# Performance work log

Hardware: AMD Instinct MI355X
Metric: run time of the kernel (lower is better)

The kernel has to match this reference:

```python
import jax, jax.numpy as jnp
import numpy as np

NUM_CHOICES = 12
NUM_LAYERS = 32
LSTM_SIZE = 2048
TEMPERATURE = 5.0
TANH_CONSTANT = 2.5


def setup_inputs() -> dict:
    key = jax.random.key(0)
    ks = jax.random.split(key, 6)
    H, C = LSTM_SIZE, NUM_CHOICES
    u = lambda k, shape: jax.random.uniform(k, shape, jnp.float32, -0.1, 0.1)
    return {
        "prev_c": jnp.zeros((1, H), jnp.float32),
        "prev_h": jnp.zeros((1, H), jnp.float32),
        "encoder": u(ks[0], (C, H)),
        "w_ih": u(ks[1], (4 * H, H)),
        "w_hh": u(ks[2], (4 * H, H)),
        "b_ih": u(ks[3], (4 * H,)),
        "b_hh": u(ks[4], (4 * H,)),
        "w_soft": u(ks[5], (C, H)),
    }


def _rollout(prev_c, prev_h, encoder, w_ih, w_hh, b_ih, b_hh, w_soft):
    keys = jax.random.split(jax.random.key(42), NUM_LAYERS)
    x0 = encoder[0][None, :]  # inputs = encoder(zeros(1).long())

    def step(carry, key):
        c, h, x = carry
        # torch LSTMCell: gates = x W_ih^T + b_ih + h W_hh^T + b_hh; order i,f,g,o
        gates = x @ w_ih.T + b_ih + h @ w_hh.T + b_hh  # [1, 4H]
        i, f, g, o = jnp.split(gates, 4, axis=-1)
        c2 = jax.nn.sigmoid(f) * c + jax.nn.sigmoid(i) * jnp.tanh(g)
        h2 = jax.nn.sigmoid(o) * jnp.tanh(c2)
        logits = (h2 @ w_soft.T) / TEMPERATURE
        logits = TANH_CONSTANT * jnp.tanh(logits)  # [1, C]
        logp = jax.nn.log_softmax(logits, axis=-1)
        op = jax.random.categorical(key, logits[0])  # scalar int, ~ multinomial(prob,1)
        nll = -logp[0, op]  # F.cross_entropy(logits, op_id), batch=1
        ent = jax.lax.stop_gradient(-jnp.sum(jnp.exp(logp) * logp))
        x_next = encoder[op + 1][None, :]  # note: op+1 gather (clamped at table edge)
        return (c2, h2, x_next), (op, nll, ent)

    (_, _, _), (op_seq, nlls, ents) = jax.lax.scan(step, (prev_c, prev_h, x0), keys)
    return op_seq, jnp.sum(nlls), jnp.sum(ents)


def reference(prev_c, prev_h, encoder, w_ih, w_hh, b_ih, b_hh, w_soft):
    return _rollout(prev_c, prev_h, encoder, w_ih, w_hh, b_ih, b_hh, w_soft)
```

## Files before the change

### kernel.cpp

```cpp
#include <hip/hip_runtime.h>
#include <stdint.h>

#define HDIM 2048
#define NC   12
#define NL   32
#define NBLK 256
#define NTHR 512
#define NWAVE 8
#define SPINCAP 2000000
#define TAG(t) (0x600D0000u | (uint32_t)(t))

__device__ __forceinline__ uint32_t rotl32(uint32_t x, int r) {
  return (x << r) | (x >> (32 - r));
}
__device__ __forceinline__ void tf2x32(uint32_t k0, uint32_t k1,
                                       uint32_t &x0, uint32_t &x1) {
  const uint32_t ks2 = k0 ^ k1 ^ 0x1BD11BDAu;
  x0 += k0; x1 += k1;
#define TFR(r) { x0 += x1; x1 = rotl32(x1, (r)); x1 ^= x0; }
  TFR(13) TFR(15) TFR(26) TFR(6)   x0 += k1;  x1 += ks2 + 1u;
  TFR(17) TFR(29) TFR(16) TFR(24)  x0 += ks2; x1 += k0  + 2u;
  TFR(13) TFR(15) TFR(26) TFR(6)   x0 += k0;  x1 += k1  + 3u;
  TFR(17) TFR(29) TFR(16) TFR(24)  x0 += k1;  x1 += ks2 + 4u;
  TFR(13) TFR(15) TFR(26) TFR(6)   x0 += ks2; x1 += k0  + 5u;
#undef TFR
}

__device__ __forceinline__ uint64_t ald64(const uint64_t* p) {
  return __hip_atomic_load(p, __ATOMIC_RELAXED, __HIP_MEMORY_SCOPE_AGENT);
}
__device__ __forceinline__ void ast64(uint64_t* p, uint64_t v) {
  __hip_atomic_store(p, v, __ATOMIC_RELAXED, __HIP_MEMORY_SCOPE_AGENT);
}
#define CFENCE() asm volatile("" ::: "memory")

__global__ void __launch_bounds__(NTHR, 2) ctrl_kernel(
    const float* __restrict__ prev_c, const float* __restrict__ prev_h,
    const float* __restrict__ encoder, const float* __restrict__ w_ih,
    const float* __restrict__ w_hh, const float* __restrict__ b_ih,
    const float* __restrict__ b_hh, const float* __restrict__ w_soft,
    float* __restrict__ out, float* __restrict__ ws)
{
  const int tid  = threadIdx.x;
  const int lane = tid & 63;
  const int wv   = tid >> 6;
  const int blk  = blockIdx.x;
  const int j    = blk * NWAVE + wv;

  uint64_t* hb = (uint64_t*)ws;

  __shared__ __align__(16) float s_h[HDIM];
  __shared__ float s_E[NWAVE][4][NC];
  __shared__ float s_dot[16];
  __shared__ int   s_op;

  if (tid < 16) s_dot[tid] = 0.f;

  {
    float4 wif[4][8];
    #pragma unroll
    for (int g = 0; g < 4; ++g) {
      const float4* wp = reinterpret_cast<const float4*>(w_ih + (size_t)(g * HDIM + j) * HDIM);
      #pragma unroll
      for (int k = 0; k < 8; ++k) wif[g][k] = wp[k * 64 + lane];
    }
    float bsum[4];
    #pragma unroll
    for (int g = 0; g < 4; ++g) bsum[g] = b_ih[g * HDIM + j] + b_hh[g * HDIM + j];

    for (int c = 0; c < NC; ++c) {
      const float4* ep = reinterpret_cast<const float4*>(encoder + (size_t)c * HDIM);
      float s0 = 0.f, s1 = 0.f, s2 = 0.f, s3 = 0.f;
      #pragma unroll
      for (int k = 0; k < 8; ++k) {
        float4 e = ep[k * 64 + lane];
        s0 += wif[0][k].x*e.x + wif[0][k].y*e.y + wif[0][k].z*e.z + wif[0][k].w*e.w;
        s1 += wif[1][k].x*e.x + wif[1][k].y*e.y + wif[1][k].z*e.z + wif[1][k].w*e.w;
        s2 += wif[2][k].x*e.x + wif[2][k].y*e.y + wif[2][k].z*e.z + wif[2][k].w*e.w;
        s3 += wif[3][k].x*e.x + wif[3][k].y*e.y + wif[3][k].z*e.z + wif[3][k].w*e.w;
      }
      #pragma unroll
      for (int d = 1; d < 64; d <<= 1) {
        s0 += __shfl_xor(s0, d, 64); s1 += __shfl_xor(s1, d, 64);
        s2 += __shfl_xor(s2, d, 64); s3 += __shfl_xor(s3, d, 64);
      }
      if (lane == 0) {
        s_E[wv][0][c] = s0 + bsum[0]; s_E[wv][1][c] = s1 + bsum[1];
        s_E[wv][2][c] = s2 + bsum[2]; s_E[wv][3][c] = s3 + bsum[3];
      }
    }
  }
  __syncthreads();

  float c_val   = prev_c[j];
  float nll_acc = 0.f, ent_acc = 0.f;

  for (int t = 0; t <= NL; ++t) {
    if (t == 0) {
      reinterpret_cast<float4*>(s_h)[tid] = reinterpret_cast<const float4*>(prev_h)[tid];
    } else {
      const uint64_t* base = hb + ((t - 1) & 1) * HDIM + wv * 256;
      const uint32_t want = TAG(t - 1);
      uint64_t v0 = 0, v1 = 0, v2 = 0, v3 = 0;
      for (int it = 0; it < SPINCAP; ++it) {
        v0 = ald64(base + lane);       v1 = ald64(base + lane + 64);
        v2 = ald64(base + lane + 128); v3 = ald64(base + lane + 192);
        bool ok = ((uint32_t)(v0 >> 32) == want) & ((uint32_t)(v1 >> 32) == want)
                & ((uint32_t)(v2 >> 32) == want) & ((uint32_t)(v3 >> 32) == want);
        if (__all(ok)) break;
      }
      CFENCE();
      s_h[wv * 256 + lane]       = __uint_as_float((uint32_t)v0);
      s_h[wv * 256 + lane + 64]  = __uint_as_float((uint32_t)v1);
      s_h[wv * 256 + lane + 128] = __uint_as_float((uint32_t)v2);
      s_h[wv * 256 + lane + 192] = __uint_as_float((uint32_t)v3);
    }
    __syncthreads();

    if (t > 0) {
      const int c0 = wv, c1 = wv + 8;
      const float4* sh4 = reinterpret_cast<const float4*>(s_h);
      const float4* wsA = reinterpret_cast<const float4*>(w_soft + (size_t)c0 * HDIM);
      const float4* wsB = reinterpret_cast<const float4*>(w_soft + (size_t)(c1 < NC ? c1 : 0) * HDIM);
      float d0 = 0.f, d1 = 0.f;
      #pragma unroll
      for (int k = 0; k < 8; ++k) {
        float4 h4 = sh4[k * 64 + lane];
        float4 a  = wsA[k * 64 + lane];
        d0 += a.x*h4.x + a.y*h4.y + a.z*h4.z + a.w*h4.w;
        if (c1 < NC) {
          float4 b = wsB[k * 64 + lane];
          d1 += b.x*h4.x + b.y*h4.y + b.z*h4.z + b.w*h4.w;
        }
      }
      #pragma unroll
      for (int d = 1; d < 64; d <<= 1) {
        d0 += __shfl_xor(d0, d, 64);
        d1 += __shfl_xor(d1, d, 64);
      }
      if (lane == 0) {
        s_dot[c0] = d0;
        if (c1 < NC) s_dot[c1] = d1;
      }
    }
    __syncthreads();

    if (t > 0 && wv == 0) {
      const int tt = t - 1;
      const float logit = (lane < NC) ? 2.5f * tanhf(s_dot[lane] * 0.2f) : 0.f;

      uint32_t k0, k1, bits;
      { uint32_t a = 0u, b = (uint32_t)tt;   tf2x32(0u, 42u, a, b); k0 = a; k1 = b; }
      { uint32_t a = 0u, b = (uint32_t)lane; tf2x32(k0, k1, a, b); bits = a ^ b; }
      const float TINY = 1.175494350822287508e-38f;
      float f01 = __uint_as_float((bits >> 9) | 0x3f800000u) - 1.0f;
      float u = f01 * (1.0f - TINY) + TINY;
      u = fmaxf(TINY, u);
      const float gmb = -logf(-logf(u));

      float by = (lane < NC) ? (logit + gmb) : -1e30f;
      int   bi = (lane < NC) ? lane : 999;
      #pragma unroll
      for (int d = 1; d < 16; d <<= 1) {
        float oy = __shfl_xor(by, d, 16);
        int   oi = __shfl_xor(bi, d, 16);
        if (oy > by || (oy == by && oi < bi)) { by = oy; bi = oi; }
      }
      const int op = bi;

      if (blk == 0) {
        float m = (lane < NC) ? logit : -1e30f;
        #pragma unroll
        for (int d = 1; d < 16; d <<= 1) m = fmaxf(m, __shfl_xor(m, d, 16));
        const float sh = logit - m;
        float S = (lane < NC) ? expf(sh) : 0.f;
        #pragma unroll
        for (int d = 1; d < 16; d <<= 1) S += __shfl_xor(S, d, 16);
        const float lp = sh - logf(S);
        const float lp_op = __shfl(lp, op, 16);
        float tm = (lane < NC) ? expf(lp) * lp : 0.f;
        #pragma unroll
        for (int d = 1; d < 16; d <<= 1) tm += __shfl_xor(tm, d, 16);
        if (lane == 0) {
          out[tt] = (float)op + 0.002f;
          nll_acc += -lp_op;
          ent_acc += -tm;
          if (t == NL) { out[NL] = nll_acc; out[NL + 1] = ent_acc; }
        }
      }
      if (lane == 0) s_op = op;
    }
    if (t == NL) break;

    float4 hf[8];
    #pragma unroll
    for (int k = 0; k < 8; ++k) hf[k] = reinterpret_cast<const float4*>(s_h)[k * 64 + lane];
    float gate[4];
    #pragma unroll
    for (int g = 0; g < 4; ++g) {
      const float4* wp = reinterpret_cast<const float4*>(w_hh + (size_t)(g * HDIM + j) * HDIM);
      float s = 0.f;
      #pragma unroll
      for (int k = 0; k < 8; ++k) {
        float4 b = wp[k * 64 + lane];
        s += b.x*hf[k].x + b.y*hf[k].y + b.z*hf[k].z + b.w*hf[k].w;
      }
      #pragma unroll
      for (int d = 1; d < 64; d <<= 1) s += __shfl_xor(s, d, 64);
      gate[g] = s;
    }
    __syncthreads();

    const int c_idx = (t == 0) ? 0 : ((s_op + 1 > NC - 1) ? NC - 1 : s_op + 1);

    const float iv = 1.f / (1.f + expf(-(gate[0] + s_E[wv][0][c_idx])));
    const float fv = 1.f / (1.f + expf(-(gate[1] + s_E[wv][1][c_idx])));
    const float gv = tanhf(gate[2] + s_E[wv][2][c_idx]);
    const float ov = 1.f / (1.f + expf(-(gate[3] + s_E[wv][3][c_idx])));
    c_val = fv * c_val + iv * gv;
    const float h_new = ov * tanhf(c_val);

    if (lane == 0) {
      uint64_t w = ((uint64_t)TAG(t) << 32) | (uint64_t)__float_as_uint(h_new);
      ast64(hb + (t & 1) * HDIM + j, w);
    }
  }
}

extern "C" void kernel_launch(void* const* d_in, const int* in_sizes, int n_in,
                              void* d_out, int out_size, void* d_ws, size_t ws_size,
                              hipStream_t stream) {
  const float* prev_c  = (const float*)d_in[0];
  const float* prev_h  = (const float*)d_in[1];
  const float* encoder = (const float*)d_in[2];
  const float* w_ih    = (const float*)d_in[3];
  const float* w_hh    = (const float*)d_in[4];
  const float* b_ih    = (const float*)d_in[5];
  const float* b_hh    = (const float*)d_in[6];
  const float* w_soft  = (const float*)d_in[7];
  float* out = (float*)d_out;
  float* ws  = (float*)d_ws;

  void* args[] = {&prev_c, &prev_h, &encoder, &w_ih, &w_hh, &b_ih, &b_hh, &w_soft, &out, &ws};
  hipError_t e = hipLaunchCooperativeKernel(reinterpret_cast<void*>(ctrl_kernel),
                                            dim3(NBLK), dim3(NTHR), args, 0, stream);
  if (e != hipSuccess) {
    ctrl_kernel<<<dim3(NBLK), dim3(NTHR), 0, stream>>>(prev_c, prev_h, encoder, w_ih, w_hh,
                                                       b_ih, b_hh, w_soft, out, ws);
  }
}
```

Measured before the change: 765.5 us.

## Replace tagged per-element h polling with per-block ready flags

Each block now writes its 8 new h values as plain floats and then sets a one-byte flag for that step. The flag is written only after a vmcnt wait, so the data stores are complete first. On the reader side, only wave 0 polls the 256 step flags with 32-bit loads and s_sleep backoff, and all waves then read the h vector once. This is meant to cut the heavy L2 traffic from every wave spinning on 64-bit tagged words. In exchange it adds extra block barriers and a serialized data-then-flag publish, and it relies on the flags region being zeroed for each launch.

```diff
diff --git a/kernel.cpp b/kernel.cpp
--- a/kernel.cpp
+++ b/kernel.cpp
@@ -8,7 +8,6 @@
 #define NTHR 512
 #define NWAVE 8
 #define SPINCAP 2000000
-#define TAG(t) (0x600D0000u | (uint32_t)(t))
 
 __device__ __forceinline__ uint32_t rotl32(uint32_t x, int r) {
   return (x << r) | (x >> (32 - r));
@@ -26,12 +25,19 @@
 #undef TFR
 }
 
-__device__ __forceinline__ uint64_t ald64(const uint64_t* p) {
+__device__ __forceinline__ uint32_t ald32(const uint32_t* p) {
   return __hip_atomic_load(p, __ATOMIC_RELAXED, __HIP_MEMORY_SCOPE_AGENT);
 }
-__device__ __forceinline__ void ast64(uint64_t* p, uint64_t v) {
+__device__ __forceinline__ float aldf(const float* p) {
+  return __uint_as_float(__hip_atomic_load((const uint32_t*)p, __ATOMIC_RELAXED, __HIP_MEMORY_SCOPE_AGENT));
+}
+__device__ __forceinline__ void astf(float* p, float v) {
+  __hip_atomic_store((uint32_t*)p, __float_as_uint(v), __ATOMIC_RELAXED, __HIP_MEMORY_SCOPE_AGENT);
+}
+__device__ __forceinline__ void ast8(uint8_t* p, uint8_t v) {
   __hip_atomic_store(p, v, __ATOMIC_RELAXED, __HIP_MEMORY_SCOPE_AGENT);
 }
+#define VMCNT0() asm volatile("s_waitcnt vmcnt(0)" ::: "memory")
 #define CFENCE() asm volatile("" ::: "memory")
 
 __global__ void __launch_bounds__(NTHR, 2) ctrl_kernel(
@@ -47,11 +53,13 @@
   const int blk  = blockIdx.x;
   const int j    = blk * NWAVE + wv;
 
-  uint64_t* hb = (uint64_t*)ws;
+  float*   hbF    = ws;
+  uint8_t* flags8 = (uint8_t*)(ws + 2 * HDIM);
 
   __shared__ __align__(16) float s_h[HDIM];
   __shared__ float s_E[NWAVE][4][NC];
   __shared__ float s_dot[16];
+  __shared__ float s_hnew[NWAVE];
   __shared__ int   s_op;
 
   if (tid < 16) s_dot[tid] = 0.f;
@@ -99,21 +107,25 @@
     if (t == 0) {
       reinterpret_cast<float4*>(s_h)[tid] = reinterpret_cast<const float4*>(prev_h)[tid];
     } else {
-      const uint64_t* base = hb + ((t - 1) & 1) * HDIM + wv * 256;
-      const uint32_t want = TAG(t - 1);
-      uint64_t v0 = 0, v1 = 0, v2 = 0, v3 = 0;
-      for (int it = 0; it < SPINCAP; ++it) {
-        v0 = ald64(base + lane);       v1 = ald64(base + lane + 64);
-        v2 = ald64(base + lane + 128); v3 = ald64(base + lane + 192);
-        bool ok = ((uint32_t)(v0 >> 32) == want) & ((uint32_t)(v1 >> 32) == want)
-                & ((uint32_t)(v2 >> 32) == want) & ((uint32_t)(v3 >> 32) == want);
-        if (__all(ok)) break;
-      }
-      CFENCE();
-      s_h[wv * 256 + lane]       = __uint_as_float((uint32_t)v0);
-      s_h[wv * 256 + lane + 64]  = __uint_as_float((uint32_t)v1);
-      s_h[wv * 256 + lane + 128] = __uint_as_float((uint32_t)v2);
-      s_h[wv * 256 + lane + 192] = __uint_as_float((uint32_t)v3);
+      if (wv == 0) {
+        const uint32_t* fw = (const uint32_t*)(flags8 + (size_t)(t - 1) * NBLK);
+        for (int it = 0; it < SPINCAP; ++it) {
+          uint32_t w = ald32(fw + lane);
+          if (__all(w == 0x01010101u)) break;
+          __builtin_amdgcn_s_sleep(8);
+        }
+        CFENCE();
+      }
+      __syncthreads();
+      {
+        const float* base = hbF + ((t - 1) & 1) * HDIM + wv * 256;
+        float v0 = aldf(base + lane),       v1 = aldf(base + lane + 64),
+              v2 = aldf(base + lane + 128), v3 = aldf(base + lane + 192);
+        s_h[wv * 256 + lane]       = v0;
+        s_h[wv * 256 + lane + 64]  = v1;
+        s_h[wv * 256 + lane + 128] = v2;
+        s_h[wv * 256 + lane + 192] = v3;
+      }
     }
     __syncthreads();
 
@@ -220,9 +232,12 @@
     c_val = fv * c_val + iv * gv;
     const float h_new = ov * tanhf(c_val);
 
-    if (lane == 0) {
-      uint64_t w = ((uint64_t)TAG(t) << 32) | (uint64_t)__float_as_uint(h_new);
-      ast64(hb + (t & 1) * HDIM + j, w);
+    if (lane == 0) s_hnew[wv] = h_new;
+    __syncthreads();
+    if (wv == 0) {
+      if (lane < NWAVE) astf(hbF + (t & 1) * HDIM + blk * NWAVE + lane, s_hnew[lane]);
+      VMCNT0();
+      if (lane == 0) ast8(flags8 + (size_t)t * NBLK + blk, (uint8_t)1);
     }
   }
 }
```

After: 851.8 us. 1.11x slower.
